# Performance work log

Hardware: AMD Instinct MI355X
Metric: run time of the kernel (lower is better)

The kernel has to match this reference:

```python
import jax, jax.numpy as jnp
import numpy as np


def setup_inputs() -> dict:
    key = jax.random.key(0)
    k1, k2, k3 = jax.random.split(key, 3)
    vol_shape = (4, 1, 128, 192, 192)   # [B, C, D, H, W]
    dsc_shape = (4, 1, 8, 12, 12)       # PatchGAN-style discriminator logits
    return {
        "dsc_fake": jax.random.normal(k1, dsc_shape, dtype=jnp.float32),
        "predicts": jax.random.normal(k2, vol_shape, dtype=jnp.float32),
        "y_data": jax.random.normal(k3, vol_shape, dtype=jnp.float32),
        "zeros": jnp.zeros(dsc_shape, dtype=jnp.float32),
    }


def reference(dsc_fake, predicts, y_data, zeros):
    # BCE with logits (stable form), target = zeros
    bce = jnp.mean(
        jnp.maximum(dsc_fake, 0.0) - dsc_fake * zeros
        + jnp.log1p(jnp.exp(-jnp.abs(dsc_fake)))
    )
    # L1 loss between target volume and prediction
    g_loss_l1 = jnp.mean(jnp.abs(y_data - predicts))
    # Finite-difference gradient MSE along D, H, W (axes 2,3,4).
    # Original detaches to numpy, so this term carries no gradient.
    yd = jax.lax.stop_gradient(y_data)
    pr = jax.lax.stop_gradient(predicts)
    g_loss_gd = jnp.float32(0.0)
    for ax in (2, 3, 4):
        gy = jnp.abs(jnp.gradient(yd, axis=ax))   # central diff interior, one-sided edges
        gp = jnp.abs(jnp.gradient(pr, axis=ax))
        g_loss_gd = g_loss_gd + jnp.mean((gy - gp) ** 2)
    return bce + 100.0 * g_loss_l1 + 100.0 * g_loss_gd
```

## Files before the change

### kernel.cpp

```cpp
#include <hip/hip_runtime.h>
#include <math.h>

namespace {
constexpr int BATCH = 4;
constexpr int DDIM  = 128;
constexpr int HDIM  = 192;
constexpr int WDIM  = 192;
constexpr long long NTOT = (long long)BATCH * DDIM * HDIM * WDIM;
constexpr int GW    = WDIM / 4;
constexpr int NDSC  = 4 * 1 * 8 * 12 * 12;
constexpr int TH    = 8;
constexpr int SROWS = TH + 2;
constexpr int SGRP  = SROWS * GW;
constexpr int SFL   = SGRP * 4;
constexpr int BLOCK = TH * GW;
constexpr int NWAVE = BLOCK / 64;
constexpr int NCHUNK = (SGRP + 63) / 64;
constexpr int DC    = 16;
constexpr int GRID  = BATCH * (HDIM / TH) * (DDIM / DC);
}

__device__ __forceinline__ float4 ld4(const float* __restrict__ p, long long g) {
    return *(const float4*)(p + 4LL * g);
}

__device__ __forceinline__ void stage(const float* __restrict__ vol, long long fbase,
                                      float* lds, int wave, int lane) {
    for (int c = wave; c < NCHUNK; c += NWAVE) {
        const int gbase = (c == NCHUNK - 1) ? (SGRP - 64) : (c * 64);
        const float* g = vol + fbase + 4LL * (gbase + lane);
        __builtin_amdgcn_global_load_lds(
            (const __attribute__((address_space(1))) void*)g,
            (__attribute__((address_space(3))) void*)(lds + 4 * gbase),
            16, 0, 0);
    }
}

__global__ __launch_bounds__(BLOCK) void vol_kernel(const float* __restrict__ p,
                                                    const float* __restrict__ y,
                                                    float* __restrict__ part) {
    __shared__ __align__(16) float smem[3][2][SFL];

    int bid = blockIdx.x;
    const int dIdx = bid % (DDIM / DC); bid /= (DDIM / DC);
    const int hIdx = bid % (HDIM / TH); bid /= (HDIM / TH);
    const int b    = bid;
    const int d0   = dIdx * DC;
    const int h0   = hIdx * TH;

    const int tid  = threadIdx.x;
    const int lane = tid & 63;
    const int wave = tid >> 6;
    const int r    = tid / GW;
    const int gw   = tid % GW;
    const int h    = h0 + r;

    const int g0     = (h0 == 0) ? 0 : ((h0 == HDIM - TH) ? (HDIM - SROWS) : (h0 - 1));
    const int rowOff = h0 - g0;
    const int sf     = ((r + rowOff) * GW + gw) * 4;

    const int   hmF = ((h == 0)        ? 0 : -GW) * 4;
    const int   hpF = ((h == HDIM - 1) ? 0 :  GW) * 4;
    const float sh  = (h == 0 || h == HDIM - 1) ? 1.f : 0.5f;
    const float swx = (gw == 0)      ? 1.f : 0.5f;
    const float sww = (gw == GW - 1) ? 1.f : 0.5f;
    const bool needL = (lane == 0)  && (gw > 0);
    const bool needR = (lane == 63) && (gw < GW - 1);

    const long long planeStride = (long long)HDIM * WDIM;
    const long long volBase = (long long)b * DDIM * planeStride + (long long)g0 * WDIM;

    float* curY = &smem[0][0][0]; float* curP = &smem[0][1][0];
    float* nxtY = &smem[1][0][0]; float* nxtP = &smem[1][1][0];
    float* freY = &smem[2][0][0]; float* freP = &smem[2][1][0];

    stage(y, volBase + (long long)d0 * planeStride, curY, wave, lane);
    stage(p, volBase + (long long)d0 * planeStride, curP, wave, lane);
    stage(y, volBase + (long long)(d0 + 1) * planeStride, nxtY, wave, lane);
    stage(p, volBase + (long long)(d0 + 1) * planeStride, nxtP, wave, lane);

    const int dm = (d0 > 0) ? (d0 - 1) : 0;
    const long long gown = (((long long)b * DDIM + dm) * HDIM + h) * GW + gw;
    float4 ym = ld4(y, gown), pm = ld4(p, gown);

    float l1 = 0.f, gd = 0.f;
    float4 yc, pc;

    for (int i = 0; i < DC; ++i) {
        const int d = d0 + i;
        __syncthreads();
        if (i == 0) {
            yc = *(const float4*)(curY + sf);
            pc = *(const float4*)(curP + sf);
        }
        if (i + 2 <= DC) {
            const int dd = (d0 + i + 2 < DDIM) ? (d0 + i + 2) : (DDIM - 1);
            stage(y, volBase + (long long)dd * planeStride, freY, wave, lane);
            stage(p, volBase + (long long)dd * planeStride, freP, wave, lane);
        }

        const float4 yn  = *(const float4*)(nxtY + sf);
        const float4 pn  = *(const float4*)(nxtP + sf);
        const float4 yhm = *(const float4*)(curY + sf + hmF);
        const float4 yhp = *(const float4*)(curY + sf + hpF);
        const float4 phm = *(const float4*)(curP + sf + hmF);
        const float4 php = *(const float4*)(curP + sf + hpF);

        float Ly = __shfl_up(yc.w, 1, 64);
        float Lp = __shfl_up(pc.w, 1, 64);
        float Ry = __shfl_down(yc.x, 1, 64);
        float Rp = __shfl_down(pc.x, 1, 64);
        if (needL) { Ly = curY[sf - 1]; Lp = curP[sf - 1]; }
        if (needR) { Ry = curY[sf + 4]; Rp = curP[sf + 4]; }
        Ly = gw ? Ly : yc.x;             Lp = gw ? Lp : pc.x;
        Ry = (gw == GW - 1) ? yc.w : Ry; Rp = (gw == GW - 1) ? pc.w : Rp;

        const float sd = (d == 0 || d == DDIM - 1) ? 1.f : 0.5f;

        l1 += fabsf(yc.x - pc.x) + fabsf(yc.y - pc.y)
            + fabsf(yc.z - pc.z) + fabsf(yc.w - pc.w);

        float t0, gy, gp;
        gy = (yc.y - Ly) * swx;    gp = (pc.y - Lp) * swx;
        t0 = fabsf(gy) - fabsf(gp); gd += t0 * t0;
        gy = (yc.z - yc.x) * 0.5f; gp = (pc.z - pc.x) * 0.5f;
        t0 = fabsf(gy) - fabsf(gp); gd += t0 * t0;
        gy = (yc.w - yc.y) * 0.5f; gp = (pc.w - pc.y) * 0.5f;
        t0 = fabsf(gy) - fabsf(gp); gd += t0 * t0;
        gy = (Ry - yc.z) * sww;    gp = (Rp - pc.z) * sww;
        t0 = fabsf(gy) - fabsf(gp); gd += t0 * t0;

        t0 = fabsf((yhp.x - yhm.x) * sh) - fabsf((php.x - phm.x) * sh); gd += t0 * t0;
        t0 = fabsf((yhp.y - yhm.y) * sh) - fabsf((php.y - phm.y) * sh); gd += t0 * t0;
        t0 = fabsf((yhp.z - yhm.z) * sh) - fabsf((php.z - phm.z) * sh); gd += t0 * t0;
        t0 = fabsf((yhp.w - yhm.w) * sh) - fabsf((php.w - phm.w) * sh); gd += t0 * t0;

        t0 = fabsf((yn.x - ym.x) * sd) - fabsf((pn.x - pm.x) * sd); gd += t0 * t0;
        t0 = fabsf((yn.y - ym.y) * sd) - fabsf((pn.y - pm.y) * sd); gd += t0 * t0;
        t0 = fabsf((yn.z - ym.z) * sd) - fabsf((pn.z - pm.z) * sd); gd += t0 * t0;
        t0 = fabsf((yn.w - ym.w) * sd) - fabsf((pn.w - pm.w) * sd); gd += t0 * t0;

        ym = yc; yc = yn; pm = pc; pc = pn;
        float* tY = curY; curY = nxtY; nxtY = freY; freY = tY;
        float* tP = curP; curP = nxtP; nxtP = freP; freP = tP;
    }

    __shared__ float red1[NWAVE], red2[NWAVE];
    #pragma unroll
    for (int off = 32; off > 0; off >>= 1) {
        l1 += __shfl_down(l1, off, 64);
        gd += __shfl_down(gd, off, 64);
    }
    if (lane == 0) { red1[wave] = l1; red2[wave] = gd; }
    __syncthreads();
    if (tid == 0) {
        float s1 = 0.f, s2 = 0.f;
        #pragma unroll
        for (int w = 0; w < NWAVE; ++w) { s1 += red1[w]; s2 += red2[w]; }
        part[2 * blockIdx.x]     = s1;
        part[2 * blockIdx.x + 1] = s2;
    }
}

__global__ __launch_bounds__(256) void finalize_kernel(const float* __restrict__ dsc,
                                                       const float* __restrict__ part,
                                                       float* __restrict__ out) {
    float l1 = 0.f, gd = 0.f, s = 0.f;
    for (int i = threadIdx.x; i < GRID; i += 256) {
        l1 += part[2 * i];
        gd += part[2 * i + 1];
    }
    for (int i = threadIdx.x; i < NDSC; i += 256) {
        const float x = dsc[i];
        s += fmaxf(x, 0.f) + log1pf(expf(-fabsf(x)));
    }
    __shared__ float a[4], c[4], e[4];
    #pragma unroll
    for (int off = 32; off > 0; off >>= 1) {
        l1 += __shfl_down(l1, off, 64);
        gd += __shfl_down(gd, off, 64);
        s  += __shfl_down(s,  off, 64);
    }
    if ((threadIdx.x & 63) == 0) {
        const int w = threadIdx.x >> 6;
        a[w] = l1; c[w] = gd; e[w] = s;
    }
    __syncthreads();
    if (threadIdx.x == 0) {
        const float bce = (e[0] + e[1] + e[2] + e[3]) / (float)NDSC;
        const float l1m = (a[0] + a[1] + a[2] + a[3]) / (float)NTOT;
        const float gdm = (c[0] + c[1] + c[2] + c[3]) / (float)NTOT;
        out[0] = bce + 100.f * (l1m + gdm);
    }
}

extern "C" void kernel_launch(void* const* d_in, const int* in_sizes, int n_in,
                              void* d_out, int out_size, void* d_ws, size_t ws_size,
                              hipStream_t stream) {
    const float* dsc_fake = (const float*)d_in[0];
    const float* predicts = (const float*)d_in[1];
    const float* y_data   = (const float*)d_in[2];
    float* part = (float*)d_ws;
    float* out  = (float*)d_out;

    vol_kernel<<<GRID, BLOCK, 0, stream>>>(predicts, y_data, part);
    finalize_kernel<<<1, 256, 0, stream>>>(dsc_fake, part, out);
}
```

Baseline: 197.1 us.

## Restructure depth pipeline with fixed-count vmcnt waits and 512-thread load waves

The block grows to 512 threads so each of the 8 waves issues exactly one global-to-LDS load chunk for y and one for p per plane; only the first 384 threads compute. The generic __syncthreads is replaced by explicit s_waitcnt vmcnt(2) plus s_barrier, so the next plane's loads stay in flight while the current plane is consumed. The D-direction difference is shifted by one iteration so it uses only LDS planes already resident, and the loop runs one extra iteration to finish it. This aims to overlap loads with compute and cut barrier stalls, at the cost of idle compute lanes and reliance on hand-written waitcnt correctness.

```diff
diff --git a/kernel.cpp b/kernel.cpp
--- a/kernel.cpp
+++ b/kernel.cpp
@@ -13,9 +13,10 @@
 constexpr int SROWS = TH + 2;
 constexpr int SGRP  = SROWS * GW;
 constexpr int SFL   = SGRP * 4;
-constexpr int BLOCK = TH * GW;
+constexpr int BLOCK = 512;
 constexpr int NWAVE = BLOCK / 64;
 constexpr int NCHUNK = (SGRP + 63) / 64;
+constexpr int NCOMP = TH * GW;
 constexpr int DC    = 16;
 constexpr int GRID  = BATCH * (HDIM / TH) * (DDIM / DC);
 }
@@ -24,21 +25,23 @@
     return *(const float4*)(p + 4LL * g);
 }
 
-__device__ __forceinline__ void stage(const float* __restrict__ vol, long long fbase,
-                                      float* lds, int wave, int lane) {
-    for (int c = wave; c < NCHUNK; c += NWAVE) {
-        const int gbase = (c == NCHUNK - 1) ? (SGRP - 64) : (c * 64);
-        const float* g = vol + fbase + 4LL * (gbase + lane);
-        __builtin_amdgcn_global_load_lds(
-            (const __attribute__((address_space(1))) void*)g,
-            (__attribute__((address_space(3))) void*)(lds + 4 * gbase),
-            16, 0, 0);
-    }
-}
-
-__global__ __launch_bounds__(BLOCK) void vol_kernel(const float* __restrict__ p,
-                                                    const float* __restrict__ y,
-                                                    float* __restrict__ part) {
+__device__ __forceinline__ void stage2(const float* __restrict__ y,
+                                       const float* __restrict__ p,
+                                       long long fbase,
+                                       float* ldsY, float* ldsP,
+                                       int wave, int lane) {
+    const int gbase = (wave == NCHUNK - 1) ? (SGRP - 64) : (wave * 64);
+    __builtin_amdgcn_global_load_lds(
+        (const __attribute__((address_space(1))) void*)(y + fbase + 4LL * (gbase + lane)),
+        (__attribute__((address_space(3))) void*)(ldsY + 4 * gbase), 16, 0, 0);
+    __builtin_amdgcn_global_load_lds(
+        (const __attribute__((address_space(1))) void*)(p + fbase + 4LL * (gbase + lane)),
+        (__attribute__((address_space(3))) void*)(ldsP + 4 * gbase), 16, 0, 0);
+}
+
+__global__ __launch_bounds__(BLOCK, 6) void vol_kernel(const float* __restrict__ p,
+                                                       const float* __restrict__ y,
+                                                       float* __restrict__ part) {
     __shared__ __align__(16) float smem[3][2][SFL];
 
     int bid = blockIdx.x;
@@ -51,98 +54,103 @@
     const int tid  = threadIdx.x;
     const int lane = tid & 63;
     const int wave = tid >> 6;
-    const int r    = tid / GW;
-    const int gw   = tid % GW;
-    const int h    = h0 + r;
-
-    const int g0     = (h0 == 0) ? 0 : ((h0 == HDIM - TH) ? (HDIM - SROWS) : (h0 - 1));
+    const bool comp = (tid < NCOMP);
+
+    const int g0 = (h0 == 0) ? 0 : ((h0 == HDIM - TH) ? (HDIM - SROWS) : (h0 - 1));
+    const long long planeStride = (long long)HDIM * WDIM;
+    const long long volBase = (long long)b * DDIM * planeStride + (long long)g0 * WDIM;
+
+    stage2(y, p, volBase + (long long)d0 * planeStride,
+           &smem[0][0][0], &smem[0][1][0], wave, lane);
+    stage2(y, p, volBase + (long long)(d0 + 1) * planeStride,
+           &smem[1][0][0], &smem[1][1][0], wave, lane);
+
+    const int r  = tid / GW;
+    const int gw = tid % GW;
+    const int h  = h0 + r;
     const int rowOff = h0 - g0;
-    const int sf     = ((r + rowOff) * GW + gw) * 4;
-
-    const int   hmF = ((h == 0)        ? 0 : -GW) * 4;
-    const int   hpF = ((h == HDIM - 1) ? 0 :  GW) * 4;
+    const int sf  = ((r + rowOff) * GW + gw) * 4;
+    const int hmF = ((h == 0)        ? 0 : -GW) * 4;
+    const int hpF = ((h == HDIM - 1) ? 0 :  GW) * 4;
     const float sh  = (h == 0 || h == HDIM - 1) ? 1.f : 0.5f;
     const float swx = (gw == 0)      ? 1.f : 0.5f;
     const float sww = (gw == GW - 1) ? 1.f : 0.5f;
     const bool needL = (lane == 0)  && (gw > 0);
     const bool needR = (lane == 63) && (gw < GW - 1);
 
-    const long long planeStride = (long long)HDIM * WDIM;
-    const long long volBase = (long long)b * DDIM * planeStride + (long long)g0 * WDIM;
-
-    float* curY = &smem[0][0][0]; float* curP = &smem[0][1][0];
-    float* nxtY = &smem[1][0][0]; float* nxtP = &smem[1][1][0];
-    float* freY = &smem[2][0][0]; float* freP = &smem[2][1][0];
-
-    stage(y, volBase + (long long)d0 * planeStride, curY, wave, lane);
-    stage(p, volBase + (long long)d0 * planeStride, curP, wave, lane);
-    stage(y, volBase + (long long)(d0 + 1) * planeStride, nxtY, wave, lane);
-    stage(p, volBase + (long long)(d0 + 1) * planeStride, nxtP, wave, lane);
-
-    const int dm = (d0 > 0) ? (d0 - 1) : 0;
-    const long long gown = (((long long)b * DDIM + dm) * HDIM + h) * GW + gw;
-    float4 ym = ld4(y, gown), pm = ld4(p, gown);
+    float4 cm2y, cm1y, cm2p, cm1p;
+    if (comp) {
+        const int dm = (d0 > 0) ? (d0 - 1) : 0;
+        const long long gown = (((long long)b * DDIM + dm) * HDIM + h) * GW + gw;
+        cm1y = ld4(y, gown); cm1p = ld4(p, gown);
+    }
 
     float l1 = 0.f, gd = 0.f;
-    float4 yc, pc;
-
-    for (int i = 0; i < DC; ++i) {
-        const int d = d0 + i;
-        __syncthreads();
-        if (i == 0) {
-            yc = *(const float4*)(curY + sf);
-            pc = *(const float4*)(curP + sf);
+
+    for (int i = 0; i <= DC; ++i) {
+        if (i < DC) asm volatile("s_waitcnt vmcnt(2) lgkmcnt(0)" ::: "memory");
+        else        asm volatile("s_waitcnt vmcnt(0) lgkmcnt(0)" ::: "memory");
+        asm volatile("s_barrier" ::: "memory");
+
+        if (i + 2 <= DC) {
+            int dd = d0 + i + 2; if (dd > DDIM - 1) dd = DDIM - 1;
+            const int s = (i + 2) % 3;
+            stage2(y, p, volBase + (long long)dd * planeStride,
+                   &smem[s][0][0], &smem[s][1][0], wave, lane);
         }
-        if (i + 2 <= DC) {
-            const int dd = (d0 + i + 2 < DDIM) ? (d0 + i + 2) : (DDIM - 1);
-            stage(y, volBase + (long long)dd * planeStride, freY, wave, lane);
-            stage(p, volBase + (long long)dd * planeStride, freP, wave, lane);
+
+        if (comp) {
+            const float* curY = &smem[i % 3][0][0];
+            const float* curP = &smem[i % 3][1][0];
+            const float4 c0y = *(const float4*)(curY + sf);
+            const float4 c0p = *(const float4*)(curP + sf);
+
+            if (i >= 1) {
+                const int q = d0 + i - 1;
+                const float sd = (q == 0 || q == DDIM - 1) ? 1.f : 0.5f;
+                float t0;
+                t0 = fabsf((c0y.x - cm2y.x) * sd) - fabsf((c0p.x - cm2p.x) * sd); gd += t0 * t0;
+                t0 = fabsf((c0y.y - cm2y.y) * sd) - fabsf((c0p.y - cm2p.y) * sd); gd += t0 * t0;
+                t0 = fabsf((c0y.z - cm2y.z) * sd) - fabsf((c0p.z - cm2p.z) * sd); gd += t0 * t0;
+                t0 = fabsf((c0y.w - cm2y.w) * sd) - fabsf((c0p.w - cm2p.w) * sd); gd += t0 * t0;
+            }
+
+            if (i < DC) {
+                l1 += fabsf(c0y.x - c0p.x) + fabsf(c0y.y - c0p.y)
+                    + fabsf(c0y.z - c0p.z) + fabsf(c0y.w - c0p.w);
+
+                float Ly = __shfl_up(c0y.w, 1, 64);
+                float Lp = __shfl_up(c0p.w, 1, 64);
+                float Ry = __shfl_down(c0y.x, 1, 64);
+                float Rp = __shfl_down(c0p.x, 1, 64);
+                if (needL) { Ly = curY[sf - 1]; Lp = curP[sf - 1]; }
+                if (needR) { Ry = curY[sf + 4]; Rp = curP[sf + 4]; }
+                Ly = gw ? Ly : c0y.x;             Lp = gw ? Lp : c0p.x;
+                Ry = (gw == GW - 1) ? c0y.w : Ry; Rp = (gw == GW - 1) ? c0p.w : Rp;
+
+                float t0, gy, gp;
+                gy = (c0y.y - Ly) * swx;    gp = (c0p.y - Lp) * swx;
+                t0 = fabsf(gy) - fabsf(gp); gd += t0 * t0;
+                gy = (c0y.z - c0y.x) * 0.5f; gp = (c0p.z - c0p.x) * 0.5f;
+                t0 = fabsf(gy) - fabsf(gp); gd += t0 * t0;
+                gy = (c0y.w - c0y.y) * 0.5f; gp = (c0p.w - c0p.y) * 0.5f;
+                t0 = fabsf(gy) - fabsf(gp); gd += t0 * t0;
+                gy = (Ry - c0y.z) * sww;    gp = (Rp - c0p.z) * sww;
+                t0 = fabsf(gy) - fabsf(gp); gd += t0 * t0;
+
+                const float4 yhm = *(const float4*)(curY + sf + hmF);
+                const float4 yhp = *(const float4*)(curY + sf + hpF);
+                const float4 phm = *(const float4*)(curP + sf + hmF);
+                const float4 php = *(const float4*)(curP + sf + hpF);
+                t0 = fabsf((yhp.x - yhm.x) * sh) - fabsf((php.x - phm.x) * sh); gd += t0 * t0;
+                t0 = fabsf((yhp.y - yhm.y) * sh) - fabsf((php.y - phm.y) * sh); gd += t0 * t0;
+                t0 = fabsf((yhp.z - yhm.z) * sh) - fabsf((php.z - phm.z) * sh); gd += t0 * t0;
+                t0 = fabsf((yhp.w - yhm.w) * sh) - fabsf((php.w - phm.w) * sh); gd += t0 * t0;
+            }
+
+            cm2y = cm1y; cm1y = c0y;
+            cm2p = cm1p; cm1p = c0p;
         }
-
-        const float4 yn  = *(const float4*)(nxtY + sf);
-        const float4 pn  = *(const float4*)(nxtP + sf);
-        const float4 yhm = *(const float4*)(curY + sf + hmF);
-        const float4 yhp = *(const float4*)(curY + sf + hpF);
-        const float4 phm = *(const float4*)(curP + sf + hmF);
-        const float4 php = *(const float4*)(curP + sf + hpF);
-
-        float Ly = __shfl_up(yc.w, 1, 64);
-        float Lp = __shfl_up(pc.w, 1, 64);
-        float Ry = __shfl_down(yc.x, 1, 64);
-        float Rp = __shfl_down(pc.x, 1, 64);
-        if (needL) { Ly = curY[sf - 1]; Lp = curP[sf - 1]; }
-        if (needR) { Ry = curY[sf + 4]; Rp = curP[sf + 4]; }
-        Ly = gw ? Ly : yc.x;             Lp = gw ? Lp : pc.x;
-        Ry = (gw == GW - 1) ? yc.w : Ry; Rp = (gw == GW - 1) ? pc.w : Rp;
-
-        const float sd = (d == 0 || d == DDIM - 1) ? 1.f : 0.5f;
-
-        l1 += fabsf(yc.x - pc.x) + fabsf(yc.y - pc.y)
-            + fabsf(yc.z - pc.z) + fabsf(yc.w - pc.w);
-
-        float t0, gy, gp;
-        gy = (yc.y - Ly) * swx;    gp = (pc.y - Lp) * swx;
-        t0 = fabsf(gy) - fabsf(gp); gd += t0 * t0;
-        gy = (yc.z - yc.x) * 0.5f; gp = (pc.z - pc.x) * 0.5f;
-        t0 = fabsf(gy) - fabsf(gp); gd += t0 * t0;
-        gy = (yc.w - yc.y) * 0.5f; gp = (pc.w - pc.y) * 0.5f;
-        t0 = fabsf(gy) - fabsf(gp); gd += t0 * t0;
-        gy = (Ry - yc.z) * sww;    gp = (Rp - pc.z) * sww;
-        t0 = fabsf(gy) - fabsf(gp); gd += t0 * t0;
-
-        t0 = fabsf((yhp.x - yhm.x) * sh) - fabsf((php.x - phm.x) * sh); gd += t0 * t0;
-        t0 = fabsf((yhp.y - yhm.y) * sh) - fabsf((php.y - phm.y) * sh); gd += t0 * t0;
-        t0 = fabsf((yhp.z - yhm.z) * sh) - fabsf((php.z - phm.z) * sh); gd += t0 * t0;
-        t0 = fabsf((yhp.w - yhm.w) * sh) - fabsf((php.w - phm.w) * sh); gd += t0 * t0;
-
-        t0 = fabsf((yn.x - ym.x) * sd) - fabsf((pn.x - pm.x) * sd); gd += t0 * t0;
-        t0 = fabsf((yn.y - ym.y) * sd) - fabsf((pn.y - pm.y) * sd); gd += t0 * t0;
-        t0 = fabsf((yn.z - ym.z) * sd) - fabsf((pn.z - pm.z) * sd); gd += t0 * t0;
-        t0 = fabsf((yn.w - ym.w) * sd) - fabsf((pn.w - pm.w) * sd); gd += t0 * t0;
-
-        ym = yc; yc = yn; pm = pc; pc = pn;
-        float* tY = curY; curY = nxtY; nxtY = freY; freY = tY;
-        float* tP = curP; curP = nxtP; nxtP = freP; freP = tP;
     }
 
     __shared__ float red1[NWAVE], red2[NWAVE];
```

After: 194.2 us. No clear change (-1.5%).
